# Performance work log

Measured on AMD Instinct MI355X. Metric: run time of the kernel, lower is better.

The kernel has to match this reference:

```python
import jax, jax.numpy as jnp
import numpy as np

# Mamba2(d_model=256, headdim=32) defaults: d_state=128, d_conv=4, expand=2, ngroups=1, chunk=256
B, CIN, L = 8, 256, 1024
D_MODEL = CIN
D_INNER = 2 * D_MODEL            # expand=2 -> 512
HEADDIM = 32
NHEADS = D_INNER // HEADDIM      # 16
D_STATE = 128
D_CONV = 4
CONV_DIM = D_INNER + 2 * D_STATE             # 768 (ngroups=1)
D_IN_PROJ = 2 * D_INNER + 2 * D_STATE + NHEADS  # 1296
GN_GROUPS = 8
CHUNK = 256
EPS = 1e-5

def setup_inputs():
    key = jax.random.key(0)
    ks = jax.random.split(key, 8)
    x = jax.random.normal(ks[0], (B, CIN, L), jnp.float32)
    W_in = jax.random.normal(ks[1], (D_IN_PROJ, D_MODEL), jnp.float32) * 0.02
    conv_w = jax.random.normal(ks[2], (CONV_DIM, D_CONV), jnp.float32) * 0.2
    conv_b = jax.random.normal(ks[3], (CONV_DIM,), jnp.float32) * 0.02
    dt = jnp.exp(jax.random.uniform(ks[4], (NHEADS,)) * (jnp.log(0.1) - jnp.log(0.001)) + jnp.log(0.001))
    dt_bias = dt + jnp.log(-jnp.expm1(-dt))   # inverse softplus
    A_log = jnp.log(jax.random.uniform(ks[5], (NHEADS,), minval=1.0, maxval=16.0))
    Dp = jnp.ones((NHEADS,), jnp.float32)
    rms_w = jnp.ones((D_INNER,), jnp.float32)
    W_out = jax.random.normal(ks[6], (D_MODEL, D_INNER), jnp.float32) * 0.02
    gn_w = jnp.ones((CIN,), jnp.float32)
    gn_b = jnp.zeros((CIN,), jnp.float32)
    return dict(x=x, W_in=W_in, conv_w=conv_w, conv_b=conv_b, dt_bias=dt_bias,
                A_log=A_log, Dp=Dp, rms_w=rms_w, W_out=W_out, gn_w=gn_w, gn_b=gn_b)

def segsum(a):
    # a: (..., T) -> (..., T, T) with sum_{j<i<=t} a_i on/below diagonal, -inf above
    T = a.shape[-1]
    cs = jnp.cumsum(a, -1)
    d = cs[..., :, None] - cs[..., None, :]
    mask = jnp.tril(jnp.ones((T, T), bool))
    return jnp.where(mask, d, -jnp.inf)

def ssd(X, A, Bm, Cm):
    # X: (b,l,h,p) already dt-scaled; A: (b,l,h) = dt*A_cont; Bm,Cm: (b,l,n) (ngroups=1)
    b, l, h, p = X.shape
    n = Bm.shape[-1]
    c = l // CHUNK
    X = X.reshape(b, c, CHUNK, h, p)
    A = A.reshape(b, c, CHUNK, h).transpose(0, 3, 1, 2)      # (b,h,c,l)
    Bm = Bm.reshape(b, c, CHUNK, n)
    Cm = Cm.reshape(b, c, CHUNK, n)
    A_cs = jnp.cumsum(A, -1)                                  # (b,h,c,l)
    Lmat = jnp.exp(segsum(A))                                 # (b,h,c,l,l)
    Y_diag = jnp.einsum('bcln,bcsn,bhcls,bcshp->bclhp', Cm, Bm, Lmat, X)
    decay_states = jnp.exp(A_cs[..., -1:] - A_cs)             # (b,h,c,l)
    states = jnp.einsum('bcln,bhcl,bclhp->bchpn', Bm, decay_states, X)
    decay_chunk = jnp.exp(segsum(jnp.pad(A_cs[..., -1], ((0, 0), (0, 0), (1, 0)))))  # (b,h,c+1,c+1)
    states = jnp.concatenate([jnp.zeros_like(states[:, :1]), states], axis=1)        # (b,c+1,h,p,n)
    prev = jnp.einsum('bhzc,bchpn->bzhpn', decay_chunk, states)[:, :-1]              # (b,c,h,p,n)
    Y_off = jnp.einsum('bcln,bchpn,bhcl->bclhp', Cm, prev, jnp.exp(A_cs))
    return (Y_diag + Y_off).reshape(b, l, h, p)

def _forward(x, W_in, conv_w, conv_b, dt_bias, A_log, Dp, rms_w, W_out, gn_w, gn_b):
    u = jnp.transpose(x, (0, 2, 1))                           # (B,L,d_model)
    zxbcdt = u @ W_in.T                                       # (B,L,1296)
    z = zxbcdt[..., :D_INNER]
    xBC = zxbcdt[..., D_INNER:D_INNER + CONV_DIM]
    dt = jax.nn.softplus(zxbcdt[..., D_INNER + CONV_DIM:] + dt_bias)  # (B,L,H)
    # causal depthwise conv1d + SiLU
    xpad = jnp.pad(xBC, ((0, 0), (D_CONV - 1, 0), (0, 0)))
    xconv = conv_b + sum(conv_w[:, k] * xpad[:, k:k + L, :] for k in range(D_CONV))
    xconv = jax.nn.silu(xconv)
    xs = xconv[..., :D_INNER].reshape(B, L, NHEADS, HEADDIM)
    Bm = xconv[..., D_INNER:D_INNER + D_STATE]
    Cm = xconv[..., D_INNER + D_STATE:]
    A = -jnp.exp(A_log)                                       # (H,)
    Y = ssd(dt[..., None] * xs, dt * A, Bm, Cm)               # (B,L,H,P)
    Y = Y + xs * Dp[None, None, :, None]
    # gated RMSNorm (norm_before_gate=False): rmsnorm(y * silu(z)) * weight
    y = Y.reshape(B, L, D_INNER) * jax.nn.silu(z)
    y = y * jax.lax.rsqrt(jnp.mean(y * y, -1, keepdims=True) + EPS) * rms_w
    out = jnp.transpose(y @ W_out.T, (0, 2, 1))               # (B,C,L)
    # GroupNorm(8, C) over (channels_per_group, L)
    og = out.reshape(B, GN_GROUPS, CIN // GN_GROUPS, L)
    mu = og.mean((2, 3), keepdims=True)
    var = og.var((2, 3), keepdims=True)
    out = ((og - mu) * jax.lax.rsqrt(var + EPS)).reshape(B, CIN, L)
    out = out * gn_w[None, :, None] + gn_b[None, :, None]
    return out * jnp.tanh(jax.nn.softplus(out))               # Mish

def reference(x, W_in, conv_w, conv_b, dt_bias, A_log, Dp, rms_w, W_out, gn_w, gn_b):
    return _forward(x, W_in, conv_w, conv_b, dt_bias, A_log, Dp, rms_w, W_out, gn_w, gn_b)
```

## Files before the change

### kernel.cpp

```cpp
#include <hip/hip_runtime.h>
#include <hip/hip_bf16.h>
#include <math.h>

#define B_ 8
#define L_ 1024
#define DM 256
#define DI 512
#define HD 32
#define NH 16
#define DS 128
#define CDIM 768
#define NZX 1280
#define CH 256
#define NC 4
#define M_ (B_*L_)
#define EPSV 1e-5f

typedef short bf16x8 __attribute__((ext_vector_type(8)));
typedef float f32x4 __attribute__((ext_vector_type(4)));

#define OFF_ZX   0
#define SZ_ZX    (M_*NZX/2)
#define OFF_XC   (OFF_ZX+SZ_ZX)
#define SZ_XC    (M_*CDIM/2)
#define OFF_DT   (OFF_XC+SZ_XC)
#define SZ_DT    (M_*NH)
#define OFF_ACS  (OFF_DT+SZ_DT)
#define SZ_ACS   (B_*NC*NH*CH)
#define OFF_S0   (OFF_ACS+SZ_ACS)
#define SZ_S0    (B_*NC*CH*CH/2)
#define OFF_ST   (OFF_S0+SZ_S0)
#define SZ_ST    (B_*NC*NH*HD*DS/2)
#define OFF_Y    (OFF_ST+SZ_ST)
#define SZ_Y     (M_*DI/2)
#define OFF_YNB  (OFF_Y+SZ_Y)
#define SZ_YNB   (M_*DI/2)
#define OFF_XBF  (OFF_YNB+SZ_YNB)
#define SZ_XBF   (M_*DM/2)
#define OFF_WBF  (OFF_XBF+SZ_XBF)
#define SZ_WBF   (1296*DM/2)
#define OFF_WOBF (OFF_WBF+SZ_WBF)
#define SZ_WOBF  (DM*DI/2)
#define OFF_GNP  (OFF_WOBF+SZ_WOBF)
#define SZ_GNP   (64*2)
#define OFF_BT   (OFF_GNP+SZ_GNP)
#define SZ_BT    (32*128*256/2)
#define OFF_OUTB (OFF_BT+SZ_BT)
#define SZ_OUTB  (M_*DM/2)

__device__ __forceinline__ ushort f2bf(float v) {
  __hip_bfloat16 h = __float2bfloat16(v);
  return *(ushort*)&h;
}
__device__ __forceinline__ float bf2f(ushort u) {
  return __uint_as_float(((unsigned int)u) << 16);
}

__global__ __launch_bounds__(256) void k_prep(const float* __restrict__ x,
                                              const float* __restrict__ W_in,
                                              const float* __restrict__ W_out,
                                              const float* __restrict__ dt_bias,
                                              ushort* __restrict__ xbf,
                                              ushort* __restrict__ wbf,
                                              ushort* __restrict__ wobf,
                                              float2* __restrict__ gnp,
                                              float* __restrict__ dtb) {
  __shared__ float Ts[64][65];
  __shared__ float Xs[256][16];
  __shared__ float Ws[16][257];
  const int bid = blockIdx.x;
  const int t = threadIdx.x;
  if (bid < 512) {
    const int kt = bid & 3, lt = (bid >> 2) & 15, b = bid >> 6;
    const int k0 = kt*64, l0 = lt*64;
    for (int i = t; i < 4096; i += 256) {
      int kk = i>>6, ll = i&63;
      Ts[kk][ll] = x[(size_t)b*DM*L_ + (size_t)(k0+kk)*L_ + l0+ll];
    }
    __syncthreads();
    for (int i = t; i < 4096; i += 256) {
      int mm = i>>6, kk = i&63;
      xbf[(size_t)(b*L_ + l0+mm)*DM + k0+kk] = f2bf(Ts[kk][mm]);
    }
  } else if (bid < 512 + 1296) {
    int i = (bid-512)*256 + t;
    if (i < 1296*DM) wbf[i] = f2bf(W_in[i]);
  } else if (bid < 512 + 1296 + 512) {
    int i = (bid-512-1296)*256 + t;
    wobf[i] = f2bf(W_out[i]);
  } else if (bid == 2320) {
    if (t < 64) gnp[t] = make_float2(0.f, 0.f);
  } else {
    const int bm = (bid - 2321)*16;
    const int b = bm >> 10, l0 = bm & 1023;
    for (int i = t; i < 4096; i += 256) {
      int h = i>>8, k = i&255;
      Ws[h][k] = W_in[(size_t)(NZX+h)*DM + k];
    }
    for (int i = t; i < 4096; i += 256) {
      int k = i>>4, li = i&15;
      Xs[k][li] = x[(size_t)b*DM*L_ + (size_t)k*L_ + l0+li];
    }
    __syncthreads();
    const int h = t&15, li = t>>4;
    float acc = 0.f;
#pragma unroll 8
    for (int k = 0; k < 256; ++k) acc += Xs[k][li]*Ws[h][k];
    float v = acc + dt_bias[h];
    dtb[(size_t)bm*NH + t] = (v > 20.f) ? v : log1pf(expf(v));
  }
}

__global__ __launch_bounds__(256) void k_gemm_in_mfma(const ushort* __restrict__ xbf,
                                                      const ushort* __restrict__ wbf,
                                                      ushort* __restrict__ zxb) {
  __shared__ ushort As[2][128*40];
  __shared__ ushort Bs[2][128*40];
  const int tid = threadIdx.x;
  const int n0 = blockIdx.x*128, m0 = blockIdx.y*128;
  const int wave = tid>>6, lane = tid&63;
  const int lr = lane&15, quad = lane>>4;
  f32x4 acc[2][8];
#pragma unroll
  for (int mi=0;mi<2;++mi)
#pragma unroll
    for (int ni=0;ni<8;++ni)
#pragma unroll
      for (int r=0;r<4;++r) acc[mi][ni][r] = 0.f;
  const int srow = tid>>1, sc = (tid&1)*16;
  auto LOAD = [&](int buf, int k0) {
    *(uint4*)&As[buf][srow*40 + sc]     = *(const uint4*)(xbf + (size_t)(m0+srow)*DM + k0 + sc);
    *(uint4*)&As[buf][srow*40 + sc + 8] = *(const uint4*)(xbf + (size_t)(m0+srow)*DM + k0 + sc + 8);
    *(uint4*)&Bs[buf][srow*40 + sc]     = *(const uint4*)(wbf + (size_t)(n0+srow)*DM + k0 + sc);
    *(uint4*)&Bs[buf][srow*40 + sc + 8] = *(const uint4*)(wbf + (size_t)(n0+srow)*DM + k0 + sc + 8);
  };
  LOAD(0, 0);
#pragma unroll
  for (int i = 0; i < 8; ++i) {
    __syncthreads();
    if (i < 7) LOAD((i+1)&1, (i+1)*32);
    const int cur = i&1;
    bf16x8 af[2], bfr[8];
    af[0] = *(const bf16x8*)&As[cur][(wave*32+lr)*40 + quad*8];
    af[1] = *(const bf16x8*)&As[cur][(wave*32+16+lr)*40 + quad*8];
#pragma unroll
    for (int ni=0;ni<8;++ni) bfr[ni] = *(const bf16x8*)&Bs[cur][(ni*16+lr)*40 + quad*8];
#pragma unroll
    for (int mi=0;mi<2;++mi)
#pragma unroll
      for (int ni=0;ni<8;++ni)
        acc[mi][ni] = __builtin_amdgcn_mfma_f32_16x16x32_bf16(af[mi], bfr[ni], acc[mi][ni], 0, 0, 0);
  }
#pragma unroll
  for (int mi=0;mi<2;++mi) {
    int m = m0 + wave*32 + mi*16 + quad*4;
#pragma unroll
    for (int ni=0;ni<8;++ni) {
      int n = n0 + ni*16 + lr;
#pragma unroll
      for (int r=0;r<4;++r) zxb[(size_t)(m+r)*NZX + n] = f2bf(acc[mi][ni][r]);
    }
  }
}

__global__ __launch_bounds__(256) void k_conv(const ushort* __restrict__ zxb,
                                              const float* __restrict__ cw,
                                              const float* __restrict__ cb,
                                              ushort* __restrict__ xcb,
                                              ushort* __restrict__ btg) {
  const int j = blockIdx.x*256 + threadIdx.x;
  const int m8 = blockIdx.y*8;
  const int l0 = m8 & 1023;
  const int mb = m8 & ~1023;
  const float4 w = *(const float4*)&cw[j*4];
  const float bias = cb[j];
  float v[11];
#pragma unroll
  for (int i = 0; i < 11; ++i) {
    int ll = l0 - 3 + i;
    v[i] = (ll >= 0) ? bf2f(zxb[(size_t)(mb+ll)*NZX + DI + j]) : 0.f;
  }
  union { ushort u[8]; uint4 q; } res;
#pragma unroll
  for (int i = 0; i < 8; ++i) {
    float a = bias + w.x*v[i] + w.y*v[i+1] + w.z*v[i+2] + w.w*v[i+3];
    a = a / (1.f + expf(-a));
    res.u[i] = f2bf(a);
    xcb[(size_t)(mb+l0+i)*CDIM + j] = res.u[i];
  }
  if (j >= DI && j < DI+DS) {
    const int n = j - DI;
    const int bc = (mb >> 10)*NC + (l0 >> 8);
    const int lc = l0 & 255;
    *(uint4*)&btg[((size_t)bc*DS + n)*CH + lc] = res.q;
  }
}

__global__ __launch_bounds__(256) void k_s0_mfma(const ushort* __restrict__ xcb,
                                                 ushort* __restrict__ S0b) {
  const int lt = blockIdx.x, st = blockIdx.y, bc = blockIdx.z;
  if (st > lt) return;
  const int base = bc*CH;
  const int t = threadIdx.x;
  const int wave = t>>6, lane = t&63, lr = lane&15, quad = lane>>4;
  const int l = lt*64 + wave*16 + lr;
  f32x4 acc[4];
#pragma unroll
  for (int nt = 0; nt < 4; ++nt)
#pragma unroll
    for (int r = 0; r < 4; ++r) acc[nt][r] = 0.f;
#pragma unroll
  for (int ks = 0; ks < 4; ++ks) {
    bf16x8 af = *(const bf16x8*)(xcb + (size_t)(base+l)*CDIM + (DI+DS) + ks*32 + quad*8);
#pragma unroll
    for (int nt = 0; nt < 4; ++nt) {
      bf16x8 bf = *(const bf16x8*)(xcb + (size_t)(base + st*64 + nt*16 + lr)*CDIM + DI + ks*32 + quad*8);
      acc[nt] = __builtin_amdgcn_mfma_f32_16x16x32_bf16(af, bf, acc[nt], 0, 0, 0);
    }
  }
#pragma unroll
  for (int nt = 0; nt < 4; ++nt)
#pragma unroll
    for (int r = 0; r < 4; ++r)
      S0b[((size_t)bc*CH + lt*64 + wave*16 + quad*4 + r)*CH + st*64 + nt*16 + lr] = f2bf(acc[nt][r]);
}

__global__ __launch_bounds__(256) void k_states_mfma(const ushort* __restrict__ xcb,
                                                     const ushort* __restrict__ btg,
                                                     const float* __restrict__ dtb,
                                                     const float* __restrict__ A_log,
                                                     float* __restrict__ acs_g,
                                                     ushort* __restrict__ stb) {
  __shared__ float acs[CH];
  __shared__ ushort Xw[32][264];
  const int t = threadIdx.x;
  const int bc = blockIdx.x, h = blockIdx.y;
  const int base = bc*CH;
  float dt_t = dtb[(size_t)(base+t)*NH + h];
  float An = -expf(A_log[h]);
  acs[t] = dt_t * An;
  __syncthreads();
  for (int off = 1; off < CH; off <<= 1) {
    float v = (t >= off) ? acs[t-off] : 0.f;
    __syncthreads();
    acs[t] += v;
    __syncthreads();
  }
  float alast = acs[CH-1];
  acs_g[((size_t)bc*NH + h)*CH + t] = acs[t];
  float w = expf(alast - acs[t]) * dt_t;
  {
    const ushort* xp = xcb + (size_t)(base+t)*CDIM + h*HD;
    ushort tmp[32];
    *(uint4*)&tmp[0]  = *(const uint4*)(xp);
    *(uint4*)&tmp[8]  = *(const uint4*)(xp+8);
    *(uint4*)&tmp[16] = *(const uint4*)(xp+16);
    *(uint4*)&tmp[24] = *(const uint4*)(xp+24);
#pragma unroll
    for (int p = 0; p < 32; ++p) Xw[p][t] = f2bf(bf2f(tmp[p]) * w);
  }
  __syncthreads();
  const int wave = t>>6, lane = t&63, lr = lane&15, quad = lane>>4;
  f32x4 acc[2][2];
#pragma unroll
  for (int mt=0;mt<2;++mt)
#pragma unroll
    for (int nt=0;nt<2;++nt)
#pragma unroll
      for (int r=0;r<4;++r) acc[mt][nt][r] = 0.f;
  const ushort* bp = btg + (size_t)bc*DS*CH;
#pragma unroll
  for (int k0 = 0; k0 < CH; k0 += 32) {
    bf16x8 a0 = *(const bf16x8*)&Xw[lr][k0 + quad*8];
    bf16x8 a1 = *(const bf16x8*)&Xw[16+lr][k0 + quad*8];
    bf16x8 b0 = *(const bf16x8*)(bp + (size_t)(wave*32 + lr)*CH + k0 + quad*8);
    bf16x8 b1 = *(const bf16x8*)(bp + (size_t)(wave*32 + 16 + lr)*CH + k0 + quad*8);
    acc[0][0] = __builtin_amdgcn_mfma_f32_16x16x32_bf16(a0, b0, acc[0][0], 0,0,0);
    acc[0][1] = __builtin_amdgcn_mfma_f32_16x16x32_bf16(a0, b1, acc[0][1], 0,0,0);
    acc[1][0] = __builtin_amdgcn_mfma_f32_16x16x32_bf16(a1, b0, acc[1][0], 0,0,0);
    acc[1][1] = __builtin_amdgcn_mfma_f32_16x16x32_bf16(a1, b1, acc[1][1], 0,0,0);
  }
  size_t sb = ((size_t)bc*NH + h)*HD*DS;
#pragma unroll
  for (int mt = 0; mt < 2; ++mt)
#pragma unroll
    for (int nt = 0; nt < 2; ++nt)
#pragma unroll
      for (int r = 0; r < 4; ++r)
        stb[sb + (size_t)(mt*16 + quad*4 + r)*DS + wave*32 + nt*16 + lr] = f2bf(acc[mt][nt][r]);
}

__global__ __launch_bounds__(256) void k_y_mfma(const ushort* __restrict__ xcb,
    const float* __restrict__ dtb, const float* __restrict__ acs_g,
    const ushort* __restrict__ S0b, const ushort* __restrict__ stb,
    const float* __restrict__ Dp, ushort* __restrict__ Yb) {
  __shared__ ushort Xt[32][280];
  __shared__ float acs[CH];
  __shared__ float dts[CH];
  __shared__ float E8[CH];
  const int t = threadIdx.x;
  const int bc = blockIdx.x, h = blockIdx.y;
  const int base = bc*CH;
  const int cc = bc & 3, bc4 = bc & ~3;
  acs[t] = acs_g[((size_t)bc*NH + h)*CH + t];
  dts[t] = dtb[(size_t)(base+t)*NH + h];
  {
    const ushort* xp = xcb + (size_t)(base+t)*CDIM + h*HD;
    ushort tmp[32];
    *(uint4*)&tmp[0]  = *(const uint4*)(xp);
    *(uint4*)&tmp[8]  = *(const uint4*)(xp+8);
    *(uint4*)&tmp[16] = *(const uint4*)(xp+16);
    *(uint4*)&tmp[24] = *(const uint4*)(xp+24);
#pragma unroll
    for (int p = 0; p < 32; ++p) Xt[p][t] = tmp[p];
  }
  __syncthreads();
  E8[t] = expf(acs[t & ~7] - acs[t]) * dts[t];
  __syncthreads();
  const int wave = t>>6, lane = t&63, lr = lane&15, quad = lane>>4;
  f32x4 acc[4][2];
#pragma unroll
  for (int mt=0;mt<4;++mt)
#pragma unroll
    for (int nt=0;nt<2;++nt)
#pragma unroll
      for (int r=0;r<4;++r) acc[mt][nt][r] = 0.f;
  if (cc > 0) {
    float fj[3];
    {
      float cum = 0.f;
      for (int j = cc-1; j >= 0; --j) {
        fj[j] = expf(cum);
        cum += acs_g[((size_t)(bc4+j)*NH + h)*CH + (CH-1)];
      }
    }
#pragma unroll
    for (int ks = 0; ks < 4; ++ks) {
      bf16x8 bfr[2];
#pragma unroll
      for (int nt = 0; nt < 2; ++nt) {
        float P[8];
#pragma unroll
        for (int jj = 0; jj < 8; ++jj) P[jj] = 0.f;
        for (int j = 0; j < cc; ++j) {
          bf16x8 sv = *(const bf16x8*)(stb + ((size_t)(bc4+j)*NH + h)*HD*DS
                                       + (size_t)(nt*16+lr)*DS + ks*32 + quad*8);
#pragma unroll
          for (int jj = 0; jj < 8; ++jj) P[jj] += fj[j]*bf2f((ushort)sv[jj]);
        }
        bf16x8 bb;
#pragma unroll
        for (int jj = 0; jj < 8; ++jj) bb[jj] = (short)f2bf(P[jj]);
        bfr[nt] = bb;
      }
#pragma unroll
      for (int mt = 0; mt < 4; ++mt) {
        int l = wave*64 + mt*16 + lr;
        bf16x8 af = *(const bf16x8*)(xcb + (size_t)(base+l)*CDIM + (DI+DS) + ks*32 + quad*8);
        acc[mt][0] = __builtin_amdgcn_mfma_f32_16x16x32_bf16(af, bfr[0], acc[mt][0], 0,0,0);
        acc[mt][1] = __builtin_amdgcn_mfma_f32_16x16x32_bf16(af, bfr[1], acc[mt][1], 0,0,0);
      }
    }
#pragma unroll
    for (int mt = 0; mt < 4; ++mt)
#pragma unroll
      for (int r = 0; r < 4; ++r) {
        float e = expf(acs[wave*64 + mt*16 + quad*4 + r]);
        acc[mt][0][r] *= e;
        acc[mt][1][r] *= e;
      }
  }
  float al[4];
#pragma unroll
  for (int mt = 0; mt < 4; ++mt) al[mt] = acs[wave*64 + mt*16 + lr];
  const int km3 = 2*wave + 1;
  for (int ks = 0; ks <= km3; ++ks) {
    const int sq = ks*32 + quad*8;
    const float as0 = acs[sq];
    const float4 e0 = *(const float4*)&E8[sq];
    const float4 e1 = *(const float4*)&E8[sq+4];
    const bf16x8 xb0 = *(const bf16x8*)&Xt[lr][sq];
    const bf16x8 xb1 = *(const bf16x8*)&Xt[16+lr][sq];
    const float ev[8] = {e0.x,e0.y,e0.z,e0.w,e1.x,e1.y,e1.z,e1.w};
#pragma unroll
    for (int mt = 0; mt < 4; ++mt) {
      if (ks > ((wave*64 + mt*16 + 15) >> 5)) continue;
      const int l = wave*64 + mt*16 + lr;
      const bf16x8 sb = *(const bf16x8*)(S0b + ((size_t)bc*CH + l)*CH + sq);
      const float el = expf(al[mt] - as0);
      bf16x8 mf;
#pragma unroll
      for (int j = 0; j < 8; ++j) {
        float v = (sq + j <= l) ? bf2f((ushort)sb[j]) * el * ev[j] : 0.f;
        mf[j] = (short)f2bf(v);
      }
      acc[mt][0] = __builtin_amdgcn_mfma_f32_16x16x32_bf16(mf, xb0, acc[mt][0], 0,0,0);
      acc[mt][1] = __builtin_amdgcn_mfma_f32_16x16x32_bf16(mf, xb1, acc[mt][1], 0,0,0);
    }
  }
  const float dph = Dp[h];
#pragma unroll
  for (int mt = 0; mt < 4; ++mt) {
    const int lb = wave*64 + mt*16 + quad*4;
#pragma unroll
    for (int nt = 0; nt < 2; ++nt) {
      const int p = nt*16 + lr;
#pragma unroll
      for (int r = 0; r < 4; ++r) {
        float xv = bf2f(Xt[p][lb+r]);
        Yb[(size_t)(base+lb+r)*DI + h*HD + p] = f2bf(acc[mt][nt][r] + dph*xv);
      }
    }
  }
}

__global__ __launch_bounds__(256) void k_rms(const ushort* __restrict__ zxb,
                                             const ushort* __restrict__ Yb,
                                             const float* __restrict__ rw,
                                             ushort* __restrict__ yn) {
  const int m = blockIdx.x, t = threadIdx.x;
  float z0 = bf2f(zxb[(size_t)m*NZX + t]);
  float z1 = bf2f(zxb[(size_t)m*NZX + t + 256]);
  float y0 = bf2f(Yb[(size_t)m*DI + t])       * z0 / (1.f + expf(-z0));
  float y1 = bf2f(Yb[(size_t)m*DI + t + 256]) * z1 / (1.f + expf(-z1));
  float ss = y0*y0 + y1*y1;
#pragma unroll
  for (int off = 32; off > 0; off >>= 1) ss += __shfl_down(ss, off);
  __shared__ float red[4];
  __shared__ float sinv;
  if ((t & 63) == 0) red[t >> 6] = ss;
  __syncthreads();
  if (t == 0) sinv = rsqrtf((red[0]+red[1]+red[2]+red[3]) * (1.f/DI) + EPSV);
  __syncthreads();
  float inv = sinv;
  yn[(size_t)m*DI + t]       = f2bf(y0 * inv * rw[t]);
  yn[(size_t)m*DI + t + 256] = f2bf(y1 * inv * rw[t+256]);
}

__global__ __launch_bounds__(256) void k_gemm_out_mfma(const ushort* __restrict__ ynbf,
                                                       const ushort* __restrict__ wobf,
                                                       ushort* __restrict__ outb,
                                                       float2* __restrict__ gnp) {
  __shared__ ushort As[2][128*40];
  __shared__ ushort Bs[2][64*40];
  const int tid = threadIdx.x;
  const int n0 = blockIdx.x*64, m0 = blockIdx.y*128;
  const int wave = tid>>6, lane = tid&63;
  const int lr = lane&15, quad = lane>>4;
  f32x4 acc[2][4];
#pragma unroll
  for (int mi=0;mi<2;++mi)
#pragma unroll
    for (int ni=0;ni<4;++ni)
#pragma unroll
      for (int r=0;r<4;++r) acc[mi][ni][r] = 0.f;
  const int srow = tid>>1, sc = (tid&1)*16;
  const int brow = tid>>2, bcol = (tid&3)*8;
  auto LOAD = [&](int buf, int k0) {
    *(uint4*)&As[buf][srow*40 + sc]     = *(const uint4*)(ynbf + (size_t)(m0+srow)*DI + k0 + sc);
    *(uint4*)&As[buf][srow*40 + sc + 8] = *(const uint4*)(ynbf + (size_t)(m0+srow)*DI + k0 + sc + 8);
    *(uint4*)&Bs[buf][brow*40 + bcol]   = *(const uint4*)(wobf + (size_t)(n0+brow)*DI + k0 + bcol);
  };
  LOAD(0, 0);
#pragma unroll
  for (int i = 0; i < 16; ++i) {
    __syncthreads();
    if (i < 15) LOAD((i+1)&1, (i+1)*32);
    const int cur = i&1;
    bf16x8 af[2], bfr[4];
    af[0] = *(const bf16x8*)&As[cur][(wave*32+lr)*40 + quad*8];
    af[1] = *(const bf16x8*)&As[cur][(wave*32+16+lr)*40 + quad*8];
#pragma unroll
    for (int ni=0;ni<4;++ni) bfr[ni] = *(const bf16x8*)&Bs[cur][(ni*16+lr)*40 + quad*8];
#pragma unroll
    for (int mi=0;mi<2;++mi)
#pragma unroll
      for (int ni=0;ni<4;++ni)
        acc[mi][ni] = __builtin_amdgcn_mfma_f32_16x16x32_bf16(af[mi], bfr[ni], acc[mi][ni], 0, 0, 0);
  }
  const int b = m0 >> 10, l0 = m0 & 1023;
  float s0=0.f, ss0=0.f, s1=0.f, ss1=0.f;
#pragma unroll
  for (int mi=0;mi<2;++mi) {
    int lb = l0 + wave*32 + mi*16 + quad*4;
#pragma unroll
    for (int ni=0;ni<4;++ni) {
      int n = n0 + ni*16 + lr;
      union { ushort u[4]; uint2 q; } pk;
#pragma unroll
      for (int r=0;r<4;++r) pk.u[r] = f2bf(acc[mi][ni][r]);
      *(uint2*)&outb[(size_t)b*DM*L_ + (size_t)n*L_ + lb] = pk.q;
      float ps = acc[mi][ni][0]+acc[mi][ni][1]+acc[mi][ni][2]+acc[mi][ni][3];
      float pq = acc[mi][ni][0]*acc[mi][ni][0]+acc[mi][ni][1]*acc[mi][ni][1]
               + acc[mi][ni][2]*acc[mi][ni][2]+acc[mi][ni][3]*acc[mi][ni][3];
      if (ni < 2) { s0 += ps; ss0 += pq; } else { s1 += ps; ss1 += pq; }
    }
  }
#pragma unroll
  for (int off = 32; off > 0; off >>= 1) {
    s0 += __shfl_down(s0, off); ss0 += __shfl_down(ss0, off);
    s1 += __shfl_down(s1, off); ss1 += __shfl_down(ss1, off);
  }
  __shared__ float red[4][4];
  if (lane == 0) { red[wave][0]=s0; red[wave][1]=ss0; red[wave][2]=s1; red[wave][3]=ss1; }
  __syncthreads();
  if (tid == 0) {
    float S0=0,Q0=0,S1=0,Q1=0;
#pragma unroll
    for (int wv2 = 0; wv2 < 4; ++wv2) { S0+=red[wv2][0]; Q0+=red[wv2][1]; S1+=red[wv2][2]; Q1+=red[wv2][3]; }
    int g0 = b*8 + (n0>>5);
    atomicAdd(&gnp[g0].x, S0);   atomicAdd(&gnp[g0].y, Q0);
    atomicAdd(&gnp[g0+1].x, S1); atomicAdd(&gnp[g0+1].y, Q1);
  }
}

__global__ __launch_bounds__(256) void k_gn_apply(const float2* __restrict__ gnp,
                                                  const float* __restrict__ gw,
                                                  const float* __restrict__ gb,
                                                  const ushort* __restrict__ ob,
                                                  float* __restrict__ o) {
  const int ch = blockIdx.x & 255, b = blockIdx.x >> 8;
  const int t = threadIdx.x;
  float2 p = gnp[b*8 + (ch>>5)];
  const float mean = p.x * (1.f/(32.f*L_));
  const float var  = p.y * (1.f/(32.f*L_)) - mean*mean;
  const float inv  = rsqrtf(var + EPSV);
  const float w = gw[ch], bb = gb[ch];
  size_t base = (size_t)blockIdx.x * L_;
  ushort4 v = *(const ushort4*)&ob[base + t*4];
  float r[4] = {bf2f(v.x), bf2f(v.y), bf2f(v.z), bf2f(v.w)};
#pragma unroll
  for (int j = 0; j < 4; ++j) {
    float u = (r[j] - mean) * inv * w + bb;
    float m;
    if (u > 15.f) m = u;
    else {
      float e = expf(u);
      float a = 1.f + e;
      float a2 = a*a;
      m = u * (a2 - 1.f) / (a2 + 1.f);
    }
    r[j] = m;
  }
  *(float4*)&o[base + t*4] = make_float4(r[0], r[1], r[2], r[3]);
}

extern "C" void kernel_launch(void* const* d_in, const int* in_sizes, int n_in,
                              void* d_out, int out_size, void* d_ws, size_t ws_size,
                              hipStream_t stream) {
  const float* x       = (const float*)d_in[0];
  const float* W_in    = (const float*)d_in[1];
  const float* conv_w  = (const float*)d_in[2];
  const float* conv_b  = (const float*)d_in[3];
  const float* dt_bias = (const float*)d_in[4];
  const float* A_log   = (const float*)d_in[5];
  const float* Dp      = (const float*)d_in[6];
  const float* rms_w   = (const float*)d_in[7];
  const float* W_out   = (const float*)d_in[8];
  const float* gn_w    = (const float*)d_in[9];
  const float* gn_b    = (const float*)d_in[10];
  float* out = (float*)d_out;
  float* ws  = (float*)d_ws;

  ushort* zxb   = (ushort*)(ws + OFF_ZX);
  ushort* xcb   = (ushort*)(ws + OFF_XC);
  float*  dtb   = ws + OFF_DT;
  float*  acs   = ws + OFF_ACS;
  ushort* S0b   = (ushort*)(ws + OFF_S0);
  ushort* stb   = (ushort*)(ws + OFF_ST);
  ushort* Ybb   = (ushort*)(ws + OFF_Y);
  ushort* ynbf  = (ushort*)(ws + OFF_YNB);
  ushort* xbf   = (ushort*)(ws + OFF_XBF);
  ushort* wbf   = (ushort*)(ws + OFF_WBF);
  ushort* wobf  = (ushort*)(ws + OFF_WOBF);
  float2* gnp   = (float2*)(ws + OFF_GNP);
  ushort* btg   = (ushort*)(ws + OFF_BT);
  ushort* outb  = (ushort*)(ws + OFF_OUTB);

  k_prep         <<<dim3(512+1296+512+1+512), 256, 0, stream>>>(x, W_in, W_out, dt_bias,
                                                                xbf, wbf, wobf, gnp, dtb);
  k_gemm_in_mfma <<<dim3(NZX/128, M_/128), 256, 0, stream>>>(xbf, wbf, zxb);
  k_conv         <<<dim3(3, M_/8), 256, 0, stream>>>(zxb, conv_w, conv_b, xcb, btg);
  k_s0_mfma      <<<dim3(4, 4, B_*NC), 256, 0, stream>>>(xcb, S0b);
  k_states_mfma  <<<dim3(B_*NC, NH), 256, 0, stream>>>(xcb, btg, dtb, A_log, acs, stb);
  k_y_mfma       <<<dim3(B_*NC, NH), 256, 0, stream>>>(xcb, dtb, acs, S0b, stb, Dp, Ybb);
  k_rms          <<<dim3(M_), 256, 0, stream>>>(zxb, Ybb, rms_w, ynbf);
  k_gemm_out_mfma<<<dim3(DM/64, M_/128), 256, 0, stream>>>(ynbf, wobf, outb, gnp);
  k_gn_apply     <<<dim3(B_*DM), 256, 0, stream>>>(gnp, gn_w, gn_b, outb, out);
}
```

Baseline: 192.1 us.

## Fuse chunk-state and Y kernels into sequential per-batch SSD scan; vectorize RMS

```diff
diff --git a/kernel.cpp b/kernel.cpp
--- a/kernel.cpp
+++ b/kernel.cpp
@@ -25,13 +25,9 @@
 #define SZ_XC    (M_*CDIM/2)
 #define OFF_DT   (OFF_XC+SZ_XC)
 #define SZ_DT    (M_*NH)
-#define OFF_ACS  (OFF_DT+SZ_DT)
-#define SZ_ACS   (B_*NC*NH*CH)
-#define OFF_S0   (OFF_ACS+SZ_ACS)
+#define OFF_S0   (OFF_DT+SZ_DT)
 #define SZ_S0    (B_*NC*CH*CH/2)
-#define OFF_ST   (OFF_S0+SZ_S0)
-#define SZ_ST    (B_*NC*NH*HD*DS/2)
-#define OFF_Y    (OFF_ST+SZ_ST)
+#define OFF_Y    (OFF_S0+SZ_S0)
 #define SZ_Y     (M_*DI/2)
 #define OFF_YNB  (OFF_Y+SZ_Y)
 #define SZ_YNB   (M_*DI/2)
@@ -225,191 +221,150 @@
       S0b[((size_t)bc*CH + lt*64 + wave*16 + quad*4 + r)*CH + st*64 + nt*16 + lr] = f2bf(acc[nt][r]);
 }
 
-__global__ __launch_bounds__(256) void k_states_mfma(const ushort* __restrict__ xcb,
-                                                     const ushort* __restrict__ btg,
-                                                     const float* __restrict__ dtb,
-                                                     const float* __restrict__ A_log,
-                                                     float* __restrict__ acs_g,
-                                                     ushort* __restrict__ stb) {
+__global__ __launch_bounds__(256) void k_ssd(const ushort* __restrict__ xcb,
+                                             const ushort* __restrict__ btg,
+                                             const float* __restrict__ dtb,
+                                             const float* __restrict__ A_log,
+                                             const ushort* __restrict__ S0b,
+                                             const float* __restrict__ Dp,
+                                             ushort* __restrict__ Yb) {
   __shared__ float acs[CH];
-  __shared__ ushort Xw[32][264];
+  __shared__ float E8[CH];
+  __shared__ ushort Xt[16][264];
+  __shared__ ushort Xw[16][264];
+  __shared__ ushort Pl[16][136];
   const int t = threadIdx.x;
-  const int bc = blockIdx.x, h = blockIdx.y;
-  const int base = bc*CH;
-  float dt_t = dtb[(size_t)(base+t)*NH + h];
-  float An = -expf(A_log[h]);
-  acs[t] = dt_t * An;
-  __syncthreads();
-  for (int off = 1; off < CH; off <<= 1) {
-    float v = (t >= off) ? acs[t-off] : 0.f;
-    __syncthreads();
-    acs[t] += v;
-    __syncthreads();
-  }
-  float alast = acs[CH-1];
-  acs_g[((size_t)bc*NH + h)*CH + t] = acs[t];
-  float w = expf(alast - acs[t]) * dt_t;
-  {
-    const ushort* xp = xcb + (size_t)(base+t)*CDIM + h*HD;
-    ushort tmp[32];
-    *(uint4*)&tmp[0]  = *(const uint4*)(xp);
-    *(uint4*)&tmp[8]  = *(const uint4*)(xp+8);
-    *(uint4*)&tmp[16] = *(const uint4*)(xp+16);
-    *(uint4*)&tmp[24] = *(const uint4*)(xp+24);
-#pragma unroll
-    for (int p = 0; p < 32; ++p) Xw[p][t] = f2bf(bf2f(tmp[p]) * w);
-  }
-  __syncthreads();
+  const int b = blockIdx.x, h = blockIdx.y, ph = blockIdx.z;
   const int wave = t>>6, lane = t&63, lr = lane&15, quad = lane>>4;
-  f32x4 acc[2][2];
-#pragma unroll
-  for (int mt=0;mt<2;++mt)
+  const float An = -expf(A_log[h]);
+  const float dph = Dp[h];
+  f32x4 P[2];
+#pragma unroll
+  for (int nt=0;nt<2;++nt)
+#pragma unroll
+    for (int r=0;r<4;++r) P[nt][r] = 0.f;
+
+  for (int c = 0; c < NC; ++c) {
+    const int bc = b*NC + c;
+    const int base = bc*CH;
+    __syncthreads();
+    float dt_t = dtb[(size_t)(base+t)*NH + h];
+    acs[t] = dt_t * An;
+    __syncthreads();
+    for (int off = 1; off < CH; off <<= 1) {
+      float v = (t >= off) ? acs[t-off] : 0.f;
+      __syncthreads();
+      acs[t] += v;
+      __syncthreads();
+    }
+    const float alast = acs[CH-1];
+    const float wv_t = expf(alast - acs[t]) * dt_t;
+    E8[t] = expf(acs[t & ~7] - acs[t]) * dt_t;
+    {
+      const ushort* xp = xcb + (size_t)(base+t)*CDIM + h*HD + ph*16;
+      ushort tmp[16];
+      *(uint4*)&tmp[0] = *(const uint4*)(xp);
+      *(uint4*)&tmp[8] = *(const uint4*)(xp+8);
+#pragma unroll
+      for (int p = 0; p < 16; ++p) {
+        Xt[p][t] = tmp[p];
+        Xw[p][t] = f2bf(bf2f(tmp[p]) * wv_t);
+      }
+    }
+    if (c > 0) {
+#pragma unroll
+      for (int nt = 0; nt < 2; ++nt)
+#pragma unroll
+        for (int r = 0; r < 4; ++r)
+          Pl[quad*4+r][wave*32 + nt*16 + lr] = f2bf(P[nt][r]);
+    }
+    __syncthreads();
+
+    f32x4 acc[4];
+#pragma unroll
+    for (int mt=0;mt<4;++mt)
+#pragma unroll
+      for (int r=0;r<4;++r) acc[mt][r] = 0.f;
+
+    if (c > 0) {
+#pragma unroll
+      for (int ks = 0; ks < 4; ++ks) {
+        bf16x8 bf = *(const bf16x8*)&Pl[lr][ks*32 + quad*8];
+#pragma unroll
+        for (int mt = 0; mt < 4; ++mt) {
+          int l = wave*64 + mt*16 + lr;
+          bf16x8 af = *(const bf16x8*)(xcb + (size_t)(base+l)*CDIM + (DI+DS) + ks*32 + quad*8);
+          acc[mt] = __builtin_amdgcn_mfma_f32_16x16x32_bf16(af, bf, acc[mt], 0,0,0);
+        }
+      }
+#pragma unroll
+      for (int mt = 0; mt < 4; ++mt)
+#pragma unroll
+        for (int r = 0; r < 4; ++r)
+          acc[mt][r] *= expf(acs[wave*64 + mt*16 + quad*4 + r]);
+    }
+
+    f32x4 stacc[2];
 #pragma unroll
     for (int nt=0;nt<2;++nt)
 #pragma unroll
-      for (int r=0;r<4;++r) acc[mt][nt][r] = 0.f;
-  const ushort* bp = btg + (size_t)bc*DS*CH;
-#pragma unroll
-  for (int k0 = 0; k0 < CH; k0 += 32) {
-    bf16x8 a0 = *(const bf16x8*)&Xw[lr][k0 + quad*8];
-    bf16x8 a1 = *(const bf16x8*)&Xw[16+lr][k0 + quad*8];
-    bf16x8 b0 = *(const bf16x8*)(bp + (size_t)(wave*32 + lr)*CH + k0 + quad*8);
-    bf16x8 b1 = *(const bf16x8*)(bp + (size_t)(wave*32 + 16 + lr)*CH + k0 + quad*8);
-    acc[0][0] = __builtin_amdgcn_mfma_f32_16x16x32_bf16(a0, b0, acc[0][0], 0,0,0);
-    acc[0][1] = __builtin_amdgcn_mfma_f32_16x16x32_bf16(a0, b1, acc[0][1], 0,0,0);
-    acc[1][0] = __builtin_amdgcn_mfma_f32_16x16x32_bf16(a1, b0, acc[1][0], 0,0,0);
-    acc[1][1] = __builtin_amdgcn_mfma_f32_16x16x32_bf16(a1, b1, acc[1][1], 0,0,0);
-  }
-  size_t sb = ((size_t)bc*NH + h)*HD*DS;
-#pragma unroll
-  for (int mt = 0; mt < 2; ++mt)
-#pragma unroll
-    for (int nt = 0; nt < 2; ++nt)
-#pragma unroll
-      for (int r = 0; r < 4; ++r)
-        stb[sb + (size_t)(mt*16 + quad*4 + r)*DS + wave*32 + nt*16 + lr] = f2bf(acc[mt][nt][r]);
-}
-
-__global__ __launch_bounds__(256) void k_y_mfma(const ushort* __restrict__ xcb,
-    const float* __restrict__ dtb, const float* __restrict__ acs_g,
-    const ushort* __restrict__ S0b, const ushort* __restrict__ stb,
-    const float* __restrict__ Dp, ushort* __restrict__ Yb) {
-  __shared__ ushort Xt[32][280];
-  __shared__ float acs[CH];
-  __shared__ float dts[CH];
-  __shared__ float E8[CH];
-  const int t = threadIdx.x;
-  const int bc = blockIdx.x, h = blockIdx.y;
-  const int base = bc*CH;
-  const int cc = bc & 3, bc4 = bc & ~3;
-  acs[t] = acs_g[((size_t)bc*NH + h)*CH + t];
-  dts[t] = dtb[(size_t)(base+t)*NH + h];
-  {
-    const ushort* xp = xcb + (size_t)(base+t)*CDIM + h*HD;
-    ushort tmp[32];
-    *(uint4*)&tmp[0]  = *(const uint4*)(xp);
-    *(uint4*)&tmp[8]  = *(const uint4*)(xp+8);
-    *(uint4*)&tmp[16] = *(const uint4*)(xp+16);
-    *(uint4*)&tmp[24] = *(const uint4*)(xp+24);
-#pragma unroll
-    for (int p = 0; p < 32; ++p) Xt[p][t] = tmp[p];
-  }
-  __syncthreads();
-  E8[t] = expf(acs[t & ~7] - acs[t]) * dts[t];
-  __syncthreads();
-  const int wave = t>>6, lane = t&63, lr = lane&15, quad = lane>>4;
-  f32x4 acc[4][2];
-#pragma unroll
-  for (int mt=0;mt<4;++mt)
-#pragma unroll
-    for (int nt=0;nt<2;++nt)
-#pragma unroll
-      for (int r=0;r<4;++r) acc[mt][nt][r] = 0.f;
-  if (cc > 0) {
-    float fj[3];
-    {
-      float cum = 0.f;
-      for (int j = cc-1; j >= 0; --j) {
-        fj[j] = expf(cum);
-        cum += acs_g[((size_t)(bc4+j)*NH + h)*CH + (CH-1)];
+      for (int r=0;r<4;++r) stacc[nt][r] = 0.f;
+    if (c < NC-1) {
+      const ushort* bp = btg + (size_t)bc*DS*CH;
+#pragma unroll
+      for (int k0 = 0; k0 < CH; k0 += 32) {
+        bf16x8 a0 = *(const bf16x8*)&Xw[lr][k0 + quad*8];
+        bf16x8 b0 = *(const bf16x8*)(bp + (size_t)(wave*32 + lr)*CH + k0 + quad*8);
+        bf16x8 b1 = *(const bf16x8*)(bp + (size_t)(wave*32 + 16 + lr)*CH + k0 + quad*8);
+        stacc[0] = __builtin_amdgcn_mfma_f32_16x16x32_bf16(a0, b0, stacc[0], 0,0,0);
+        stacc[1] = __builtin_amdgcn_mfma_f32_16x16x32_bf16(a0, b1, stacc[1], 0,0,0);
       }
     }
-#pragma unroll
-    for (int ks = 0; ks < 4; ++ks) {
-      bf16x8 bfr[2];
-#pragma unroll
-      for (int nt = 0; nt < 2; ++nt) {
-        float P[8];
-#pragma unroll
-        for (int jj = 0; jj < 8; ++jj) P[jj] = 0.f;
-        for (int j = 0; j < cc; ++j) {
-          bf16x8 sv = *(const bf16x8*)(stb + ((size_t)(bc4+j)*NH + h)*HD*DS
-                                       + (size_t)(nt*16+lr)*DS + ks*32 + quad*8);
-#pragma unroll
-          for (int jj = 0; jj < 8; ++jj) P[jj] += fj[j]*bf2f((ushort)sv[jj]);
+
+    float al[4];
+#pragma unroll
+    for (int mt = 0; mt < 4; ++mt) al[mt] = acs[wave*64 + mt*16 + lr];
+    const int km3 = 2*wave + 1;
+    for (int ks = 0; ks <= km3; ++ks) {
+      const int sq = ks*32 + quad*8;
+      const float as0 = acs[sq];
+      const float4 e0 = *(const float4*)&E8[sq];
+      const float4 e1 = *(const float4*)&E8[sq+4];
+      const bf16x8 xb0 = *(const bf16x8*)&Xt[lr][sq];
+      const float ev[8] = {e0.x,e0.y,e0.z,e0.w,e1.x,e1.y,e1.z,e1.w};
+#pragma unroll
+      for (int mt = 0; mt < 4; ++mt) {
+        if (ks > ((wave*64 + mt*16 + 15) >> 5)) continue;
+        const int l = wave*64 + mt*16 + lr;
+        const bf16x8 sb = *(const bf16x8*)(S0b + ((size_t)bc*CH + l)*CH + sq);
+        const float el = expf(al[mt] - as0);
+        bf16x8 mf;
+#pragma unroll
+        for (int j = 0; j < 8; ++j) {
+          float v = (sq + j <= l) ? bf2f((ushort)sb[j]) * el * ev[j] : 0.f;
+          mf[j] = (short)f2bf(v);
         }
-        bf16x8 bb;
-#pragma unroll
-        for (int jj = 0; jj < 8; ++jj) bb[jj] = (short)f2bf(P[jj]);
-        bfr[nt] = bb;
+        acc[mt] = __builtin_amdgcn_mfma_f32_16x16x32_bf16(mf, xb0, acc[mt], 0,0,0);
       }
-#pragma unroll
-      for (int mt = 0; mt < 4; ++mt) {
-        int l = wave*64 + mt*16 + lr;
-        bf16x8 af = *(const bf16x8*)(xcb + (size_t)(base+l)*CDIM + (DI+DS) + ks*32 + quad*8);
-        acc[mt][0] = __builtin_amdgcn_mfma_f32_16x16x32_bf16(af, bfr[0], acc[mt][0], 0,0,0);
-        acc[mt][1] = __builtin_amdgcn_mfma_f32_16x16x32_bf16(af, bfr[1], acc[mt][1], 0,0,0);
+    }
+
+#pragma unroll
+    for (int mt = 0; mt < 4; ++mt) {
+      const int lb = wave*64 + mt*16 + quad*4;
+#pragma unroll
+      for (int r = 0; r < 4; ++r) {
+        float xv = bf2f(Xt[lr][lb+r]);
+        Yb[(size_t)(base+lb+r)*DI + h*HD + ph*16 + lr] = f2bf(acc[mt][r] + dph*xv);
       }
     }
-#pragma unroll
-    for (int mt = 0; mt < 4; ++mt)
-#pragma unroll
-      for (int r = 0; r < 4; ++r) {
-        float e = expf(acs[wave*64 + mt*16 + quad*4 + r]);
-        acc[mt][0][r] *= e;
-        acc[mt][1][r] *= e;
-      }
-  }
-  float al[4];
-#pragma unroll
-  for (int mt = 0; mt < 4; ++mt) al[mt] = acs[wave*64 + mt*16 + lr];
-  const int km3 = 2*wave + 1;
-  for (int ks = 0; ks <= km3; ++ks) {
-    const int sq = ks*32 + quad*8;
-    const float as0 = acs[sq];
-    const float4 e0 = *(const float4*)&E8[sq];
-    const float4 e1 = *(const float4*)&E8[sq+4];
-    const bf16x8 xb0 = *(const bf16x8*)&Xt[lr][sq];
-    const bf16x8 xb1 = *(const bf16x8*)&Xt[16+lr][sq];
-    const float ev[8] = {e0.x,e0.y,e0.z,e0.w,e1.x,e1.y,e1.z,e1.w};
-#pragma unroll
-    for (int mt = 0; mt < 4; ++mt) {
-      if (ks > ((wave*64 + mt*16 + 15) >> 5)) continue;
-      const int l = wave*64 + mt*16 + lr;
-      const bf16x8 sb = *(const bf16x8*)(S0b + ((size_t)bc*CH + l)*CH + sq);
-      const float el = expf(al[mt] - as0);
-      bf16x8 mf;
-#pragma unroll
-      for (int j = 0; j < 8; ++j) {
-        float v = (sq + j <= l) ? bf2f((ushort)sb[j]) * el * ev[j] : 0.f;
-        mf[j] = (short)f2bf(v);
-      }
-      acc[mt][0] = __builtin_amdgcn_mfma_f32_16x16x32_bf16(mf, xb0, acc[mt][0], 0,0,0);
-      acc[mt][1] = __builtin_amdgcn_mfma_f32_16x16x32_bf16(mf, xb1, acc[mt][1], 0,0,0);
-    }
-  }
-  const float dph = Dp[h];
-#pragma unroll
-  for (int mt = 0; mt < 4; ++mt) {
-    const int lb = wave*64 + mt*16 + quad*4;
-#pragma unroll
-    for (int nt = 0; nt < 2; ++nt) {
-      const int p = nt*16 + lr;
-#pragma unroll
-      for (int r = 0; r < 4; ++r) {
-        float xv = bf2f(Xt[p][lb+r]);
-        Yb[(size_t)(base+lb+r)*DI + h*HD + p] = f2bf(acc[mt][nt][r] + dph*xv);
-      }
+
+    if (c < NC-1) {
+      const float eT = expf(alast);
+#pragma unroll
+      for (int nt = 0; nt < 2; ++nt)
+#pragma unroll
+        for (int r = 0; r < 4; ++r)
+          P[nt][r] = stacc[nt][r] + eT * P[nt][r];
     }
   }
 }
@@ -418,23 +373,29 @@
                                              const ushort* __restrict__ Yb,
                                              const float* __restrict__ rw,
                                              ushort* __restrict__ yn) {
-  const int m = blockIdx.x, t = threadIdx.x;
-  float z0 = bf2f(zxb[(size_t)m*NZX + t]);
-  float z1 = bf2f(zxb[(size_t)m*NZX + t + 256]);
-  float y0 = bf2f(Yb[(size_t)m*DI + t])       * z0 / (1.f + expf(-z0));
-  float y1 = bf2f(Yb[(size_t)m*DI + t + 256]) * z1 / (1.f + expf(-z1));
-  float ss = y0*y0 + y1*y1;
-#pragma unroll
-  for (int off = 32; off > 0; off >>= 1) ss += __shfl_down(ss, off);
-  __shared__ float red[4];
-  __shared__ float sinv;
-  if ((t & 63) == 0) red[t >> 6] = ss;
-  __syncthreads();
-  if (t == 0) sinv = rsqrtf((red[0]+red[1]+red[2]+red[3]) * (1.f/DI) + EPSV);
-  __syncthreads();
-  float inv = sinv;
-  yn[(size_t)m*DI + t]       = f2bf(y0 * inv * rw[t]);
-  yn[(size_t)m*DI + t + 256] = f2bf(y1 * inv * rw[t+256]);
+  const int m = blockIdx.x*4 + (threadIdx.x>>6);
+  const int lane = threadIdx.x & 63;
+  const int c0 = lane*8;
+  bf16x8 zv = *(const bf16x8*)(zxb + (size_t)m*NZX + c0);
+  bf16x8 yv = *(const bf16x8*)(Yb  + (size_t)m*DI  + c0);
+  float y[8];
+  float ss = 0.f;
+#pragma unroll
+  for (int j = 0; j < 8; ++j) {
+    float z = bf2f((ushort)zv[j]);
+    y[j] = bf2f((ushort)yv[j]) * z / (1.f + expf(-z));
+    ss += y[j]*y[j];
+  }
+#pragma unroll
+  for (int off = 1; off < 64; off <<= 1) ss += __shfl_xor(ss, off);
+  const float inv = rsqrtf(ss * (1.f/DI) + EPSV);
+  float4 w0 = *(const float4*)&rw[c0];
+  float4 w1 = *(const float4*)&rw[c0+4];
+  const float wv[8] = {w0.x,w0.y,w0.z,w0.w,w1.x,w1.y,w1.z,w1.w};
+  union { ushort u[8]; uint4 q; } pk;
+#pragma unroll
+  for (int j = 0; j < 8; ++j) pk.u[j] = f2bf(y[j] * inv * wv[j]);
+  *(uint4*)(yn + (size_t)m*DI + c0) = pk.q;
 }
 
 __global__ __launch_bounds__(256) void k_gemm_out_mfma(const ushort* __restrict__ ynbf,
@@ -565,9 +526,7 @@
   ushort* zxb   = (ushort*)(ws + OFF_ZX);
   ushort* xcb   = (ushort*)(ws + OFF_XC);
   float*  dtb   = ws + OFF_DT;
-  float*  acs   = ws + OFF_ACS;
   ushort* S0b   = (ushort*)(ws + OFF_S0);
-  ushort* stb   = (ushort*)(ws + OFF_ST);
   ushort* Ybb   = (ushort*)(ws + OFF_Y);
   ushort* ynbf  = (ushort*)(ws + OFF_YNB);
   ushort* xbf   = (ushort*)(ws + OFF_XBF);
@@ -582,9 +541,8 @@
   k_gemm_in_mfma <<<dim3(NZX/128, M_/128), 256, 0, stream>>>(xbf, wbf, zxb);
   k_conv         <<<dim3(3, M_/8), 256, 0, stream>>>(zxb, conv_w, conv_b, xcb, btg);
   k_s0_mfma      <<<dim3(4, 4, B_*NC), 256, 0, stream>>>(xcb, S0b);
-  k_states_mfma  <<<dim3(B_*NC, NH), 256, 0, stream>>>(xcb, btg, dtb, A_log, acs, stb);
-  k_y_mfma       <<<dim3(B_*NC, NH), 256, 0, stream>>>(xcb, dtb, acs, S0b, stb, Dp, Ybb);
-  k_rms          <<<dim3(M_), 256, 0, stream>>>(zxb, Ybb, rms_w, ynbf);
+  k_ssd          <<<dim3(B_, NH, 2), 256, 0, stream>>>(xcb, btg, dtb, A_log, S0b, Dp, Ybb);
+  k_rms          <<<dim3(M_/4), 256, 0, stream>>>(zxb, Ybb, rms_w, ynbf);
   k_gemm_out_mfma<<<dim3(DM/64, M_/128), 256, 0, stream>>>(ynbf, wobf, outb, gnp);
   k_gn_apply     <<<dim3(B_*DM), 256, 0, stream>>>(gnp, gn_w, gn_b, outb, out);
 }
```

Result: slower. 221.7 us (+15.4%).
